# Kernel tuning notes

Hardware: AMD Instinct MI355X
Metric: run time of the kernel (lower is better)

Reference implementation:

```python
import jax, jax.numpy as jnp
import numpy as np

D_MODEL = 512
D_STATE = 64
DT = 1.0
BATCH = 8
SEQ = 4096


def setup_inputs() -> dict:
    key = jax.random.key(0)
    ks = jax.random.split(key, 5)
    u = jax.random.normal(ks[0], (BATCH, SEQ, D_MODEL), dtype=jnp.float32)
    log_A_real = jnp.zeros((D_STATE,), dtype=jnp.float32)
    log_A_imag = 0.1 * jax.random.normal(ks[1], (D_STATE,), dtype=jnp.float32)
    B_w = 0.1 * jax.random.normal(ks[2], (2 * D_STATE, D_MODEL), dtype=jnp.float32)
    C_w = 0.1 * jax.random.normal(ks[3], (D_MODEL, 2 * D_STATE), dtype=jnp.float32)
    D_w = jnp.eye(D_MODEL, dtype=jnp.float32)
    return {"u": u, "log_A_real": log_A_real, "log_A_imag": log_A_imag,
            "B_w": B_w, "C_w": C_w, "D_w": D_w}


def reference(u, log_A_real, log_A_imag, B_w, C_w, D_w):
    # Bilinear discretization of diagonal A_c = -exp(log_A_real) + i*log_A_imag
    ar = -jnp.exp(log_A_real)
    ai = log_A_imag
    h = 0.5 * DT
    nr, ni = 1.0 + h * ar, h * ai          # numerator 1 + dt/2 * A
    dr, di = 1.0 - h * ar, -h * ai          # denominator 1 - dt/2 * A
    den = dr * dr + di * di
    Ar = (nr * dr + ni * di) / den          # Re(A_bar), shape (N,)
    Ai = (ni * dr - nr * di) / den          # Im(A_bar)

    N = log_A_real.shape[0]
    Bu = jnp.einsum('btd,nd->btn', u, B_w)  # (B, T, 2N)
    bu_re = jnp.swapaxes(Bu[..., :N], 0, 1)  # (T, B, N)
    bu_im = jnp.swapaxes(Bu[..., N:], 0, 1)

    batch = u.shape[0]
    h0 = (jnp.zeros((batch, N), u.dtype), jnp.zeros((batch, N), u.dtype))

    def step(carry, x):
        hr, hi = carry
        xr, xi = x
        nhr = Ar * hr - Ai * hi + xr        # complex multiply + add, real form
        nhi = Ar * hi + Ai * hr + xi
        return (nhr, nhi), (nhr, nhi)

    _, (hr_all, hi_all) = jax.lax.scan(step, h0, (bu_re, bu_im))
    h_cat = jnp.concatenate([hr_all, hi_all], axis=-1)   # (T, B, 2N)
    y = jnp.einsum('tbn,dn->btd', h_cat, C_w) + jnp.einsum('btd,ed->bte', u, D_w)
    return y
```

## Files before the change

kernel.cpp:

```cpp
#include <hip/hip_runtime.h>
#include <hip/hip_bf16.h>


#define D_MODEL 512
#define N2      128
#define BATCH   8
#define SEQ     4096
#define MTOT    (BATCH*SEQ)
#define LC      16
#define NC      (SEQ/LC)
#define PADW    132

#define OFFB_ABAR   0u
#define OFFB_POWTAB 512u
#define OFFB_BWPB   16384u
#define OFFB_W2B    147456u
#define OFFB_E      1048576u
#define OFFB_P      2097152u
#define OFFB_HLOC   3145728u
#define OFFB_UBF    11534336u
#define WS_NEED_UBF 45088768u

typedef __bf16  bf16x8  __attribute__((ext_vector_type(8)));
typedef float   f32x4   __attribute__((ext_vector_type(4)));
typedef unsigned short ushort8 __attribute__((ext_vector_type(8)));

__device__ __forceinline__ unsigned short f2bf(float f) {
    union { float f; unsigned int u; } v; v.f = f;
    unsigned int r = v.u + 0x7fffu + ((v.u >> 16) & 1u);
    return (unsigned short)(r >> 16);
}
__device__ __forceinline__ float bf2f(unsigned short s) {
    union { unsigned int u; float f; } v; v.u = ((unsigned int)s) << 16;
    return v.f;
}
__device__ __forceinline__ void gload_lds16(const void* g, void* l) {
    __builtin_amdgcn_global_load_lds(
        (const __attribute__((address_space(1))) void*)g,
        (__attribute__((address_space(3))) void*)l, 16, 0, 0);
}

__global__ __launch_bounds__(256) void prep_kernel(
    const float* __restrict__ lar, const float* __restrict__ lai,
    const float* __restrict__ Bw,  const float* __restrict__ Cw,
    const float* __restrict__ Dw,
    float* __restrict__ abar, float* __restrict__ powtab,
    unsigned short* __restrict__ Bwpb, unsigned short* __restrict__ W2b)
{
    int tid = blockIdx.x * blockDim.x + threadIdx.x;
    if (blockIdx.x == 0 && threadIdx.x < 64) {
        int n = threadIdx.x;
        float ar = -expf(lar[n]);
        float ai = lai[n];
        const float h = 0.5f;
        float nr = 1.f + h * ar, ni = h * ai;
        float dr = 1.f - h * ar, di = -h * ai;
        float den = dr * dr + di * di;
        float Ar = (nr * dr + ni * di) / den;
        float Ai = (ni * dr - nr * di) / den;
        abar[2 * n] = Ar; abar[2 * n + 1] = Ai;
        float pr = Ar, pi = Ai;
        for (int i = 0; i < LC; ++i) {
            powtab[i * 128 + 2 * n]     = pr;
            powtab[i * 128 + 2 * n + 1] = pi;
            float npr = pr * Ar - pi * Ai;
            float npi = pr * Ai + pi * Ar;
            pr = npr; pi = npi;
        }
    }
    int stride = gridDim.x * blockDim.x;
    for (int idx = tid; idx < N2 * D_MODEL; idx += stride) {
        int np = idx / D_MODEL, k = idx % D_MODEL;
        int src = (np & 1) ? (64 + (np >> 1)) : (np >> 1);
        Bwpb[idx] = f2bf(Bw[src * D_MODEL + k]);
    }
    for (int idx = tid; idx < D_MODEL * 640; idx += stride) {
        int d = idx / 640, k = idx % 640;
        float v;
        if (k < D_MODEL) v = Dw[d * D_MODEL + k];
        else {
            int np = k - D_MODEL;
            int src = (np & 1) ? (64 + (np >> 1)) : (np >> 1);
            v = Cw[d * N2 + src];
        }
        W2b[idx] = f2bf(v);
    }
}

__global__ __launch_bounds__(256) void gemm1_fused(
    const float* __restrict__ u, const unsigned short* __restrict__ Bwpb,
    const float* __restrict__ abar,
    unsigned short* __restrict__ Hloc, float* __restrict__ E,
    unsigned short* __restrict__ u_bf, int write_ubf)
{
    __shared__ __align__(16) unsigned short As[64 * 64];
    __shared__ __align__(16) unsigned short Bs[128 * 64];
    __shared__ __align__(16) float Hs[64 * PADW];
    const int tid  = threadIdx.x;
    const int lane = tid & 63;
    const int w    = tid >> 6;
    const int wm   = (w >> 1) * 32;
    const int wn   = (w & 1) * 64;
    const int m0   = blockIdx.x * 64;

    f32x4 acc[2][4];
#pragma unroll
    for (int i = 0; i < 2; ++i)
#pragma unroll
        for (int j = 0; j < 4; ++j)
            acc[i][j] = (f32x4){0.f, 0.f, 0.f, 0.f};

    const int tr = tid >> 3, tc = tid & 7;

    for (int k0 = 0; k0 < D_MODEL; k0 += 64) {
        __syncthreads();
#pragma unroll
        for (int q = 0; q < 4; ++q) {
            int r = q * 32 + tr;
            int cs = tc ^ (r & 7);
            gload_lds16(Bwpb + (size_t)r * D_MODEL + k0 + cs * 8,
                        (char*)Bs + (q * 256 + tid) * 16);
        }
#pragma unroll
        for (int q = 0; q < 2; ++q) {
            int r = q * 32 + tr;
            const float* src = u + (size_t)(m0 + r) * D_MODEL + k0 + tc * 8;
            float4 v0 = *(const float4*)src;
            float4 v1 = *(const float4*)(src + 4);
            ushort8 p;
            p[0] = f2bf(v0.x); p[1] = f2bf(v0.y); p[2] = f2bf(v0.z); p[3] = f2bf(v0.w);
            p[4] = f2bf(v1.x); p[5] = f2bf(v1.y); p[6] = f2bf(v1.z); p[7] = f2bf(v1.w);
            int cd = tc ^ (r & 7);
            *(ushort8*)((char*)As + r * 128 + cd * 16) = p;
            if (write_ubf)
                *(ushort8*)&u_bf[(size_t)(m0 + r) * D_MODEL + k0 + tc * 8] = p;
        }
        __syncthreads();
#pragma unroll
        for (int kk = 0; kk < 2; ++kk) {
            bf16x8 a[2], b[4];
#pragma unroll
            for (int i = 0; i < 2; ++i) {
                int row = wm + i * 16 + (lane & 15);
                int kb  = kk * 64 + ((lane >> 4) << 4);
                a[i] = *(const bf16x8*)((const char*)As + row * 128 + (kb ^ ((row & 7) << 4)));
            }
#pragma unroll
            for (int j = 0; j < 4; ++j) {
                int row = wn + j * 16 + (lane & 15);
                int kb  = kk * 64 + ((lane >> 4) << 4);
                b[j] = *(const bf16x8*)((const char*)Bs + row * 128 + (kb ^ ((row & 7) << 4)));
            }
#pragma unroll
            for (int i = 0; i < 2; ++i)
#pragma unroll
                for (int j = 0; j < 4; ++j)
                    acc[i][j] = __builtin_amdgcn_mfma_f32_16x16x32_bf16(a[i], b[j], acc[i][j], 0, 0, 0);
        }
    }

#pragma unroll
    for (int i = 0; i < 2; ++i)
#pragma unroll
        for (int j = 0; j < 4; ++j) {
            int col = wn + j * 16 + (lane & 15);
#pragma unroll
            for (int r = 0; r < 4; ++r) {
                int row = wm + i * 16 + ((lane >> 4) << 2) + r;
                Hs[row * PADW + col] = acc[i][j][r];
            }
        }
    __syncthreads();

    {
        int n  = tid & 63;
        int cl = tid >> 6;
        float2 ab = *(const float2*)&abar[2 * n];
        float hr = 0.f, hi = 0.f;
#pragma unroll
        for (int i = 0; i < LC; ++i) {
            int t = cl * LC + i;
            float xr = Hs[t * PADW + 2 * n];
            float xi = Hs[t * PADW + 2 * n + 1];
            float nhr = fmaf(ab.x, hr, fmaf(-ab.y, hi, xr));
            float nhi = fmaf(ab.x, hi, fmaf(ab.y, hr, xi));
            hr = nhr; hi = nhi;
            Hs[t * PADW + 2 * n]     = hr;
            Hs[t * PADW + 2 * n + 1] = hi;
        }
        int b  = m0 >> 12;
        int c0 = (m0 & 4095) >> 4;
        *(float2*)&E[((size_t)(b * 64 + n) * NC + c0 + cl) * 2] = make_float2(hr, hi);
    }
    __syncthreads();

#pragma unroll
    for (int q = 0; q < 2; ++q) {
        int r = q * 32 + tr;
        int cb = tc * 16;
        const float* row = &Hs[r * PADW + cb];
        ushort8 o0, o1;
#pragma unroll
        for (int j = 0; j < 8; ++j) o0[j] = f2bf(row[j]);
#pragma unroll
        for (int j = 0; j < 8; ++j) o1[j] = f2bf(row[8 + j]);
        *(ushort8*)&Hloc[(size_t)(m0 + r) * N2 + cb]     = o0;
        *(ushort8*)&Hloc[(size_t)(m0 + r) * N2 + cb + 8] = o1;
    }
}

__global__ __launch_bounds__(256) void scan_carry_par(
    const float* __restrict__ E, const float* __restrict__ abar,
    float* __restrict__ P)
{
    const int b    = blockIdx.x;
    const int wv   = threadIdx.x >> 6;
    const int lane = threadIdx.x & 63;

    for (int n = wv * 16; n < wv * 16 + 16; ++n) {
        float2 ab = *(const float2*)&abar[2 * n];
        float ar = ab.x, ai = ab.y;
        for (int k = 0; k < 4; ++k) {
            float t = ar * ar - ai * ai;  ai = 2.f * ar * ai;  ar = t;
        }
        float pr[7], pi[7];
        pr[0] = ar; pi[0] = ai;
#pragma unroll
        for (int k = 1; k < 7; ++k) {
            pr[k] = pr[k-1] * pr[k-1] - pi[k-1] * pi[k-1];
            pi[k] = 2.f * pr[k-1] * pi[k-1];
        }
        int L = lane + 1;
        float wr = 1.f, wi = 0.f;
#pragma unroll
        for (int k = 0; k < 7; ++k) if ((L >> k) & 1) {
            float t = wr * pr[k] - wi * pi[k];
            wi = wr * pi[k] + wi * pr[k]; wr = t;
        }
        const float* Eb = E + (size_t)(b * 64 + n) * NC * 2;
        float cr = 0.f, ci = 0.f;
        for (int s = 0; s < 4; ++s) {
            float2 e = *(const float2*)&Eb[(s * 64 + lane) * 2];
            float xr = e.x, xi = e.y;
#pragma unroll
            for (int k = 0; k < 6; ++k) {
                int d = 1 << k;
                float tr_ = __shfl_up(xr, (unsigned)d);
                float ti_ = __shfl_up(xi, (unsigned)d);
                if (lane >= d) {
                    xr = fmaf(pr[k], tr_, fmaf(-pi[k], ti_, xr));
                    xi = fmaf(pr[k], ti_, fmaf(pi[k], tr_, xi));
                }
            }
            float gr = fmaf(wr, cr, fmaf(-wi, ci, xr));
            float gi = fmaf(wr, ci, fmaf(wi, cr, xi));
            float exr = __shfl_up(gr, 1u);
            float exi = __shfl_up(gi, 1u);
            if (lane == 0) { exr = cr; exi = ci; }
            *(float2*)&P[(size_t)(b * NC + s * 64 + lane) * N2 + 2 * n] =
                make_float2(exr, exi);
            cr = __shfl(gr, 63);
            ci = __shfl(gi, 63);
        }
    }
}

template<bool A1BF>
__global__ __launch_bounds__(256) void gemm2_fused(
    const float* __restrict__ uf,
    const unsigned short* __restrict__ ubf,
    const unsigned short* __restrict__ Hloc,
    const unsigned short* __restrict__ W2b,
    const float* __restrict__ P,
    const float* __restrict__ powtab,
    float* __restrict__ y)
{
    __shared__ __align__(16) unsigned short As[128 * 64];
    __shared__ __align__(16) unsigned short Bs[128 * 64];
    const int tid  = threadIdx.x;
    const int lane = tid & 63;
    const int w    = tid >> 6;
    const int wm   = (w >> 1) * 64;
    const int wn   = (w & 1) * 64;
    const int m0   = blockIdx.x * 128;
    const int n0   = blockIdx.y * 128;

    f32x4 acc[4][4];
#pragma unroll
    for (int i = 0; i < 4; ++i)
#pragma unroll
        for (int j = 0; j < 4; ++j)
            acc[i][j] = (f32x4){0.f, 0.f, 0.f, 0.f};

    const int tr = tid >> 3, tc = tid & 7;

    for (int k0 = 0; k0 < 640; k0 += 64) {
        __syncthreads();
#pragma unroll
        for (int q = 0; q < 4; ++q) {
            int r = q * 32 + tr;
            int cs = tc ^ (r & 7);
            gload_lds16(W2b + (size_t)(n0 + r) * 640 + k0 + cs * 8,
                        (char*)Bs + (q * 256 + tid) * 16);
        }
        if (k0 < D_MODEL) {
            if constexpr (A1BF) {
#pragma unroll
                for (int q = 0; q < 4; ++q) {
                    int r = q * 32 + tr;
                    int cs = tc ^ (r & 7);
                    gload_lds16(ubf + (size_t)(m0 + r) * D_MODEL + k0 + cs * 8,
                                (char*)As + (q * 256 + tid) * 16);
                }
            } else {
#pragma unroll
                for (int q = 0; q < 4; ++q) {
                    int r = q * 32 + tr;
                    const float* src = uf + (size_t)(m0 + r) * D_MODEL + k0 + tc * 8;
                    float4 v0 = *(const float4*)src;
                    float4 v1 = *(const float4*)(src + 4);
                    ushort8 p;
                    p[0] = f2bf(v0.x); p[1] = f2bf(v0.y); p[2] = f2bf(v0.z); p[3] = f2bf(v0.w);
                    p[4] = f2bf(v1.x); p[5] = f2bf(v1.y); p[6] = f2bf(v1.z); p[7] = f2bf(v1.w);
                    int cd = tc ^ (r & 7);
                    *(ushort8*)((char*)As + r * 128 + cd * 16) = p;
                }
            }
        } else {
            const int kk0 = k0 - D_MODEL;
#pragma unroll
            for (int q = 0; q < 4; ++q) {
                int r = q * 32 + tr;
                int m = m0 + r;
                int b = m >> 12, t = m & 4095;
                int c = t >> 4, i = t & 15;
                ushort8 hl = *(const ushort8*)&Hloc[(size_t)m * N2 + kk0 + tc * 8];
                const float* Pp = P + (size_t)(b * NC + c) * N2 + kk0 + tc * 8;
                float4 p0 = *(const float4*)Pp;
                float4 p1 = *(const float4*)(Pp + 4);
                const float* Wp = powtab + i * 128 + kk0 + tc * 8;
                float4 w0 = *(const float4*)Wp;
                float4 w1 = *(const float4*)(Wp + 4);
                ushort8 p;
                p[0] = f2bf(fmaf(w0.x, p0.x, fmaf(-w0.y, p0.y, bf2f(hl[0]))));
                p[1] = f2bf(fmaf(w0.x, p0.y, fmaf( w0.y, p0.x, bf2f(hl[1]))));
                p[2] = f2bf(fmaf(w0.z, p0.z, fmaf(-w0.w, p0.w, bf2f(hl[2]))));
                p[3] = f2bf(fmaf(w0.z, p0.w, fmaf( w0.w, p0.z, bf2f(hl[3]))));
                p[4] = f2bf(fmaf(w1.x, p1.x, fmaf(-w1.y, p1.y, bf2f(hl[4]))));
                p[5] = f2bf(fmaf(w1.x, p1.y, fmaf( w1.y, p1.x, bf2f(hl[5]))));
                p[6] = f2bf(fmaf(w1.z, p1.z, fmaf(-w1.w, p1.w, bf2f(hl[6]))));
                p[7] = f2bf(fmaf(w1.z, p1.w, fmaf( w1.w, p1.z, bf2f(hl[7]))));
                int cd = tc ^ (r & 7);
                *(ushort8*)((char*)As + r * 128 + cd * 16) = p;
            }
        }
        __syncthreads();
#pragma unroll
        for (int kk = 0; kk < 2; ++kk) {
            bf16x8 a[4], b[4];
#pragma unroll
            for (int i = 0; i < 4; ++i) {
                int row = wm + i * 16 + (lane & 15);
                int kb  = kk * 64 + ((lane >> 4) << 4);
                a[i] = *(const bf16x8*)((const char*)As + row * 128 + (kb ^ ((row & 7) << 4)));
            }
#pragma unroll
            for (int j = 0; j < 4; ++j) {
                int row = wn + j * 16 + (lane & 15);
                int kb  = kk * 64 + ((lane >> 4) << 4);
                b[j] = *(const bf16x8*)((const char*)Bs + row * 128 + (kb ^ ((row & 7) << 4)));
            }
#pragma unroll
            for (int i = 0; i < 4; ++i)
#pragma unroll
                for (int j = 0; j < 4; ++j)
                    acc[i][j] = __builtin_amdgcn_mfma_f32_16x16x32_bf16(a[i], b[j], acc[i][j], 0, 0, 0);
        }
    }

#pragma unroll
    for (int i = 0; i < 4; ++i)
#pragma unroll
        for (int j = 0; j < 4; ++j) {
            int col = n0 + wn + j * 16 + (lane & 15);
#pragma unroll
            for (int r = 0; r < 4; ++r) {
                int row = m0 + wm + i * 16 + ((lane >> 4) << 2) + r;
                y[(size_t)row * D_MODEL + col] = acc[i][j][r];
            }
        }
}

extern "C" void kernel_launch(void* const* d_in, const int* in_sizes, int n_in,
                              void* d_out, int out_size, void* d_ws, size_t ws_size,
                              hipStream_t stream)
{
    const float* u   = (const float*)d_in[0];
    const float* lar = (const float*)d_in[1];
    const float* lai = (const float*)d_in[2];
    const float* Bw  = (const float*)d_in[3];
    const float* Cw  = (const float*)d_in[4];
    const float* Dw  = (const float*)d_in[5];
    float* y = (float*)d_out;
    char* ws = (char*)d_ws;

    float*          abar   = (float*)(ws + OFFB_ABAR);
    float*          powtab = (float*)(ws + OFFB_POWTAB);
    unsigned short* Bwpb   = (unsigned short*)(ws + OFFB_BWPB);
    unsigned short* W2b    = (unsigned short*)(ws + OFFB_W2B);
    float*          E      = (float*)(ws + OFFB_E);
    float*          P      = (float*)(ws + OFFB_P);
    unsigned short* Hloc   = (unsigned short*)(ws + OFFB_HLOC);
    unsigned short* u_bf   = (unsigned short*)(ws + OFFB_UBF);

    const int use_ubf = (ws_size >= (size_t)WS_NEED_UBF) ? 1 : 0;

    hipLaunchKernelGGL(prep_kernel, dim3(128), dim3(256), 0, stream,
                       lar, lai, Bw, Cw, Dw, abar, powtab, Bwpb, W2b);
    hipLaunchKernelGGL(gemm1_fused, dim3(MTOT / 64), dim3(256), 0, stream,
                       u, Bwpb, abar, Hloc, E, u_bf, use_ubf);
    hipLaunchKernelGGL(scan_carry_par, dim3(BATCH), dim3(256), 0, stream,
                       E, abar, P);
    if (use_ubf) {
        hipLaunchKernelGGL((gemm2_fused<true>), dim3(MTOT / 128, D_MODEL / 128),
                           dim3(256), 0, stream,
                           u, u_bf, Hloc, W2b, P, powtab, y);
    } else {
        hipLaunchKernelGGL((gemm2_fused<false>), dim3(MTOT / 128, D_MODEL / 128),
                           dim3(256), 0, stream,
                           u, u_bf, Hloc, W2b, P, powtab, y);
    }
}
```

Before: 185.7 us.

## Double-buffer LDS in both GEMMs, parallelize carry scan, drop bf16 u copy

Both GEMM kernels now use ping-pong LDS buffers, so the next K-tile is staged while the current one is computed, with one barrier per iteration instead of two. The carry scan kernel is spread over an 8x8 grid of state groups instead of 8 blocks, which should raise parallelism in that latency-bound stage. The bf16 copy of u written by gemm1 and read by gemm2 is removed, so gemm2 re-reads fp32 u and converts it itself. This saves a large write but doubles gemm2's A-side read bytes, and the larger LDS footprint may lower occupancy.

```diff
diff --git a/kernel.cpp b/kernel.cpp
--- a/kernel.cpp
+++ b/kernel.cpp
@@ -18,8 +18,6 @@
 #define OFFB_E      1048576u
 #define OFFB_P      2097152u
 #define OFFB_HLOC   3145728u
-#define OFFB_UBF    11534336u
-#define WS_NEED_UBF 45088768u
 
 typedef __bf16  bf16x8  __attribute__((ext_vector_type(8)));
 typedef float   f32x4   __attribute__((ext_vector_type(4)));
@@ -90,18 +88,22 @@
 __global__ __launch_bounds__(256) void gemm1_fused(
     const float* __restrict__ u, const unsigned short* __restrict__ Bwpb,
     const float* __restrict__ abar,
-    unsigned short* __restrict__ Hloc, float* __restrict__ E,
-    unsigned short* __restrict__ u_bf, int write_ubf)
+    unsigned short* __restrict__ Hloc, float* __restrict__ E)
 {
-    __shared__ __align__(16) unsigned short As[64 * 64];
-    __shared__ __align__(16) unsigned short Bs[128 * 64];
-    __shared__ __align__(16) float Hs[64 * PADW];
+    __shared__ __align__(16) char smem[49152];
+    unsigned short* As0 = (unsigned short*)smem;
+    unsigned short* As1 = (unsigned short*)(smem + 8192);
+    unsigned short* Bs0 = (unsigned short*)(smem + 16384);
+    unsigned short* Bs1 = (unsigned short*)(smem + 32768);
+    float* Hs = (float*)smem;
+
     const int tid  = threadIdx.x;
     const int lane = tid & 63;
     const int w    = tid >> 6;
     const int wm   = (w >> 1) * 32;
     const int wn   = (w & 1) * 64;
     const int m0   = blockIdx.x * 64;
+    const int tr = tid >> 3, tc = tid & 7;
 
     f32x4 acc[2][4];
 #pragma unroll
@@ -110,16 +112,14 @@
         for (int j = 0; j < 4; ++j)
             acc[i][j] = (f32x4){0.f, 0.f, 0.f, 0.f};
 
-    const int tr = tid >> 3, tc = tid & 7;
-
-    for (int k0 = 0; k0 < D_MODEL; k0 += 64) {
-        __syncthreads();
+    auto stage = [&](int t, unsigned short* Asb, unsigned short* Bsb) {
+        const int k0 = t * 64;
 #pragma unroll
         for (int q = 0; q < 4; ++q) {
             int r = q * 32 + tr;
             int cs = tc ^ (r & 7);
             gload_lds16(Bwpb + (size_t)r * D_MODEL + k0 + cs * 8,
-                        (char*)Bs + (q * 256 + tid) * 16);
+                        (char*)Bsb + (q * 256 + tid) * 16);
         }
 #pragma unroll
         for (int q = 0; q < 2; ++q) {
@@ -131,11 +131,10 @@
             p[0] = f2bf(v0.x); p[1] = f2bf(v0.y); p[2] = f2bf(v0.z); p[3] = f2bf(v0.w);
             p[4] = f2bf(v1.x); p[5] = f2bf(v1.y); p[6] = f2bf(v1.z); p[7] = f2bf(v1.w);
             int cd = tc ^ (r & 7);
-            *(ushort8*)((char*)As + r * 128 + cd * 16) = p;
-            if (write_ubf)
-                *(ushort8*)&u_bf[(size_t)(m0 + r) * D_MODEL + k0 + tc * 8] = p;
-        }
-        __syncthreads();
+            *(ushort8*)((char*)Asb + r * 128 + cd * 16) = p;
+        }
+    };
+    auto compute = [&](const unsigned short* Asb, const unsigned short* Bsb) {
 #pragma unroll
         for (int kk = 0; kk < 2; ++kk) {
             bf16x8 a[2], b[4];
@@ -143,13 +142,13 @@
             for (int i = 0; i < 2; ++i) {
                 int row = wm + i * 16 + (lane & 15);
                 int kb  = kk * 64 + ((lane >> 4) << 4);
-                a[i] = *(const bf16x8*)((const char*)As + row * 128 + (kb ^ ((row & 7) << 4)));
+                a[i] = *(const bf16x8*)((const char*)Asb + row * 128 + (kb ^ ((row & 7) << 4)));
             }
 #pragma unroll
             for (int j = 0; j < 4; ++j) {
                 int row = wn + j * 16 + (lane & 15);
                 int kb  = kk * 64 + ((lane >> 4) << 4);
-                b[j] = *(const bf16x8*)((const char*)Bs + row * 128 + (kb ^ ((row & 7) << 4)));
+                b[j] = *(const bf16x8*)((const char*)Bsb + row * 128 + (kb ^ ((row & 7) << 4)));
             }
 #pragma unroll
             for (int i = 0; i < 2; ++i)
@@ -157,8 +156,20 @@
                 for (int j = 0; j < 4; ++j)
                     acc[i][j] = __builtin_amdgcn_mfma_f32_16x16x32_bf16(a[i], b[j], acc[i][j], 0, 0, 0);
         }
-    }
-
+    };
+
+    unsigned short *Ac = As0, *Bc = Bs0, *An = As1, *Bn = Bs1;
+    stage(0, Ac, Bc);
+    for (int t = 0; t < 8; ++t) {
+        __syncthreads();
+        if (t + 1 < 8) stage(t + 1, An, Bn);
+        compute(Ac, Bc);
+        unsigned short* s;
+        s = Ac; Ac = An; An = s;
+        s = Bc; Bc = Bn; Bn = s;
+    }
+
+    __syncthreads();
 #pragma unroll
     for (int i = 0; i < 2; ++i)
 #pragma unroll
@@ -214,10 +225,11 @@
     float* __restrict__ P)
 {
     const int b    = blockIdx.x;
+    const int g0   = blockIdx.y * 8;
     const int wv   = threadIdx.x >> 6;
     const int lane = threadIdx.x & 63;
 
-    for (int n = wv * 16; n < wv * 16 + 16; ++n) {
+    for (int n = g0 + wv * 2; n < g0 + wv * 2 + 2; ++n) {
         float2 ab = *(const float2*)&abar[2 * n];
         float ar = ab.x, ai = ab.y;
         for (int k = 0; k < 4; ++k) {
@@ -265,18 +277,20 @@
     }
 }
 
-template<bool A1BF>
 __global__ __launch_bounds__(256) void gemm2_fused(
     const float* __restrict__ uf,
-    const unsigned short* __restrict__ ubf,
     const unsigned short* __restrict__ Hloc,
     const unsigned short* __restrict__ W2b,
     const float* __restrict__ P,
     const float* __restrict__ powtab,
     float* __restrict__ y)
 {
-    __shared__ __align__(16) unsigned short As[128 * 64];
-    __shared__ __align__(16) unsigned short Bs[128 * 64];
+    __shared__ __align__(16) char smem[65536];
+    unsigned short* As0 = (unsigned short*)smem;
+    unsigned short* As1 = (unsigned short*)(smem + 16384);
+    unsigned short* Bs0 = (unsigned short*)(smem + 32768);
+    unsigned short* Bs1 = (unsigned short*)(smem + 49152);
+
     const int tid  = threadIdx.x;
     const int lane = tid & 63;
     const int w    = tid >> 6;
@@ -284,6 +298,7 @@
     const int wn   = (w & 1) * 64;
     const int m0   = blockIdx.x * 128;
     const int n0   = blockIdx.y * 128;
+    const int tr = tid >> 3, tc = tid & 7;
 
     f32x4 acc[4][4];
 #pragma unroll
@@ -292,39 +307,27 @@
         for (int j = 0; j < 4; ++j)
             acc[i][j] = (f32x4){0.f, 0.f, 0.f, 0.f};
 
-    const int tr = tid >> 3, tc = tid & 7;
-
-    for (int k0 = 0; k0 < 640; k0 += 64) {
-        __syncthreads();
+    auto stage = [&](int t, unsigned short* Asb, unsigned short* Bsb) {
+        const int k0 = t * 64;
 #pragma unroll
         for (int q = 0; q < 4; ++q) {
             int r = q * 32 + tr;
             int cs = tc ^ (r & 7);
             gload_lds16(W2b + (size_t)(n0 + r) * 640 + k0 + cs * 8,
-                        (char*)Bs + (q * 256 + tid) * 16);
+                        (char*)Bsb + (q * 256 + tid) * 16);
         }
         if (k0 < D_MODEL) {
-            if constexpr (A1BF) {
-#pragma unroll
-                for (int q = 0; q < 4; ++q) {
-                    int r = q * 32 + tr;
-                    int cs = tc ^ (r & 7);
-                    gload_lds16(ubf + (size_t)(m0 + r) * D_MODEL + k0 + cs * 8,
-                                (char*)As + (q * 256 + tid) * 16);
-                }
-            } else {
-#pragma unroll
-                for (int q = 0; q < 4; ++q) {
-                    int r = q * 32 + tr;
-                    const float* src = uf + (size_t)(m0 + r) * D_MODEL + k0 + tc * 8;
-                    float4 v0 = *(const float4*)src;
-                    float4 v1 = *(const float4*)(src + 4);
-                    ushort8 p;
-                    p[0] = f2bf(v0.x); p[1] = f2bf(v0.y); p[2] = f2bf(v0.z); p[3] = f2bf(v0.w);
-                    p[4] = f2bf(v1.x); p[5] = f2bf(v1.y); p[6] = f2bf(v1.z); p[7] = f2bf(v1.w);
-                    int cd = tc ^ (r & 7);
-                    *(ushort8*)((char*)As + r * 128 + cd * 16) = p;
-                }
+#pragma unroll
+            for (int q = 0; q < 4; ++q) {
+                int r = q * 32 + tr;
+                const float* src = uf + (size_t)(m0 + r) * D_MODEL + k0 + tc * 8;
+                float4 v0 = *(const float4*)src;
+                float4 v1 = *(const float4*)(src + 4);
+                ushort8 p;
+                p[0] = f2bf(v0.x); p[1] = f2bf(v0.y); p[2] = f2bf(v0.z); p[3] = f2bf(v0.w);
+                p[4] = f2bf(v1.x); p[5] = f2bf(v1.y); p[6] = f2bf(v1.z); p[7] = f2bf(v1.w);
+                int cd = tc ^ (r & 7);
+                *(ushort8*)((char*)Asb + r * 128 + cd * 16) = p;
             }
         } else {
             const int kk0 = k0 - D_MODEL;
@@ -332,8 +335,8 @@
             for (int q = 0; q < 4; ++q) {
                 int r = q * 32 + tr;
                 int m = m0 + r;
-                int b = m >> 12, t = m & 4095;
-                int c = t >> 4, i = t & 15;
+                int b = m >> 12, tt = m & 4095;
+                int c = tt >> 4, i = tt & 15;
                 ushort8 hl = *(const ushort8*)&Hloc[(size_t)m * N2 + kk0 + tc * 8];
                 const float* Pp = P + (size_t)(b * NC + c) * N2 + kk0 + tc * 8;
                 float4 p0 = *(const float4*)Pp;
@@ -351,10 +354,11 @@
                 p[6] = f2bf(fmaf(w1.z, p1.z, fmaf(-w1.w, p1.w, bf2f(hl[6]))));
                 p[7] = f2bf(fmaf(w1.z, p1.w, fmaf( w1.w, p1.z, bf2f(hl[7]))));
                 int cd = tc ^ (r & 7);
-                *(ushort8*)((char*)As + r * 128 + cd * 16) = p;
-            }
-        }
-        __syncthreads();
+                *(ushort8*)((char*)Asb + r * 128 + cd * 16) = p;
+            }
+        }
+    };
+    auto compute = [&](const unsigned short* Asb, const unsigned short* Bsb) {
 #pragma unroll
         for (int kk = 0; kk < 2; ++kk) {
             bf16x8 a[4], b[4];
@@ -362,13 +366,13 @@
             for (int i = 0; i < 4; ++i) {
                 int row = wm + i * 16 + (lane & 15);
                 int kb  = kk * 64 + ((lane >> 4) << 4);
-                a[i] = *(const bf16x8*)((const char*)As + row * 128 + (kb ^ ((row & 7) << 4)));
+                a[i] = *(const bf16x8*)((const char*)Asb + row * 128 + (kb ^ ((row & 7) << 4)));
             }
 #pragma unroll
             for (int j = 0; j < 4; ++j) {
                 int row = wn + j * 16 + (lane & 15);
                 int kb  = kk * 64 + ((lane >> 4) << 4);
-                b[j] = *(const bf16x8*)((const char*)Bs + row * 128 + (kb ^ ((row & 7) << 4)));
+                b[j] = *(const bf16x8*)((const char*)Bsb + row * 128 + (kb ^ ((row & 7) << 4)));
             }
 #pragma unroll
             for (int i = 0; i < 4; ++i)
@@ -376,6 +380,17 @@
                 for (int j = 0; j < 4; ++j)
                     acc[i][j] = __builtin_amdgcn_mfma_f32_16x16x32_bf16(a[i], b[j], acc[i][j], 0, 0, 0);
         }
+    };
+
+    unsigned short *Ac = As0, *Bc = Bs0, *An = As1, *Bn = Bs1;
+    stage(0, Ac, Bc);
+    for (int t = 0; t < 10; ++t) {
+        __syncthreads();
+        if (t + 1 < 10) stage(t + 1, An, Bn);
+        compute(Ac, Bc);
+        unsigned short* s;
+        s = Ac; Ac = An; An = s;
+        s = Bc; Bc = Bn; Bn = s;
     }
 
 #pragma unroll
@@ -411,23 +426,14 @@
     float*          E      = (float*)(ws + OFFB_E);
     float*          P      = (float*)(ws + OFFB_P);
     unsigned short* Hloc   = (unsigned short*)(ws + OFFB_HLOC);
-    unsigned short* u_bf   = (unsigned short*)(ws + OFFB_UBF);
-
-    const int use_ubf = (ws_size >= (size_t)WS_NEED_UBF) ? 1 : 0;
 
     hipLaunchKernelGGL(prep_kernel, dim3(128), dim3(256), 0, stream,
                        lar, lai, Bw, Cw, Dw, abar, powtab, Bwpb, W2b);
     hipLaunchKernelGGL(gemm1_fused, dim3(MTOT / 64), dim3(256), 0, stream,
-                       u, Bwpb, abar, Hloc, E, u_bf, use_ubf);
-    hipLaunchKernelGGL(scan_carry_par, dim3(BATCH), dim3(256), 0, stream,
+                       u, Bwpb, abar, Hloc, E);
+    hipLaunchKernelGGL(scan_carry_par, dim3(8, 8), dim3(256), 0, stream,
                        E, abar, P);
-    if (use_ubf) {
-        hipLaunchKernelGGL((gemm2_fused<true>), dim3(MTOT / 128, D_MODEL / 128),
-                           dim3(256), 0, stream,
-                           u, u_bf, Hloc, W2b, P, powtab, y);
-    } else {
-        hipLaunchKernelGGL((gemm2_fused<false>), dim3(MTOT / 128, D_MODEL / 128),
-                           dim3(256), 0, stream,
-                           u, u_bf, Hloc, W2b, P, powtab, y);
-    }
-}
+    hipLaunchKernelGGL(gemm2_fused, dim3(MTOT / 128, D_MODEL / 128),
+                       dim3(256), 0, stream,
+                       u, Hloc, W2b, P, powtab, y);
+}
```

Result: faster. 175.8 us (-5.3%).
